# Optimization experiments

Hardware: AMD Instinct MI355X
Metric: run time of the kernel (lower is better)

## Reference

```python
import jax, jax.numpy as jnp
import numpy as np

B, L, DK, DV, H = 2, 2048, 512, 512, 8
DH_K = DK // H  # 64
DH_V = DV // H  # 64


def setup_inputs() -> dict:
    key = jax.random.key(0)
    ks = jax.random.split(key, 6)
    scale_w = 1.0 / np.sqrt(DK)
    return {
        "keys": jax.random.normal(ks[0], (B, L, DK), dtype=jnp.float32),
        "queries": jax.random.normal(ks[1], (B, L, DK), dtype=jnp.float32),
        "values": jax.random.normal(ks[2], (B, L, DV), dtype=jnp.float32),
        "WQ": jax.random.normal(ks[3], (H, DK, DH_K), dtype=jnp.float32) * scale_w,
        "WK": jax.random.normal(ks[4], (H, DK, DH_K), dtype=jnp.float32) * scale_w,
        "WV": jax.random.normal(ks[5], (H, DV, DH_V), dtype=jnp.float32) * scale_w,
    }


def reference(keys, queries, values, WQ, WK, WV):
    # Per-head projections, vectorized over all H heads at once.
    Q = jnp.einsum('bld,hde->bhle', queries, WQ)   # [B,H,Lq,dh]
    K = jnp.einsum('bld,hde->bhle', keys, WK)      # [B,H,Lk,dh]
    V = jnp.einsum('bld,hde->bhle', values, WV)    # [B,H,Lk,dv_h]
    Lk = keys.shape[1]
    # NOTE: original scales by sqrt(seq_len_k), not sqrt(head_dim).
    y = jnp.einsum('bhqe,bhke->bhqk', Q, K) / jnp.sqrt(jnp.float32(Lk))
    # NOTE: original applies softmax over torch dim=1 of [B,Lq,Lk],
    # i.e. the QUERY axis (axis=2 here in [B,H,Lq,Lk]).
    z = jax.nn.softmax(y, axis=2)
    out = jnp.einsum('bhqk,bhke->bhqe', z, V)      # [B,H,Lq,dv_h]
    # Concat heads on the feature dim (same order as torch.concat(..., 2)).
    Bq, Hh, Lq, Dh = out.shape
    return out.transpose(0, 2, 1, 3).reshape(Bq, Lq, Hh * Dh)
```

## Files before the change

### kernel.cpp

```cpp
#include <hip/hip_runtime.h>
#include <hip/hip_bf16.h>

#define LL 2048
#define DM 512
#define SCALE 0.02209708691207961f

typedef unsigned short u16;
typedef __attribute__((ext_vector_type(8))) short short8;
typedef __attribute__((ext_vector_type(4))) short short4v;
typedef __attribute__((ext_vector_type(4))) float f32x4;

#define XAQ_OFF 0u
#define XAK_OFF 2097152u
#define XAV_OFF 4194304u
#define WB_OFF  6291456u
#define QA_OFF  7077888u
#define KA_OFF  9175040u
#define VB_OFF  11272192u
#define S_OFF   13369344u

__device__ __forceinline__ u16 f2bf(float f) {
  union { float f; unsigned u; } v; v.f = f;
  unsigned r = v.u + 0x7fff + ((v.u >> 16) & 1);
  return (u16)(r >> 16);
}
__device__ __forceinline__ size_t frag_idx(int bh, int t64, int w, int c, int lane) {
  return ((((size_t)(bh * 32 + t64) * 4 + w) * 2 + c) * 64 + lane) * 8;
}
__device__ __forceinline__ size_t vb_idx(int bh, int kt, int w, int et, int lane) {
  return ((((size_t)(bh * 32 + kt) * 4 + w) * 4 + et) * 64 + lane) * 4;
}

__global__ __launch_bounds__(256) void prep_kernel(
    const float* __restrict__ queries, const float* __restrict__ keys,
    const float* __restrict__ values, const float* __restrict__ WQ,
    const float* __restrict__ WK, const float* __restrict__ WV,
    u16* __restrict__ wsb) {
  int t = threadIdx.x;
  int blk = blockIdx.x;
  if (blk < 768) {
    int tens = blk >> 8;
    int grp  = blk & 255;
    const float* src = (tens == 0 ? queries : tens == 1 ? keys : values) +
                       (size_t)grp * 16 * 512;
    __shared__ __align__(16) u16 Xs[16][520];
#pragma unroll
    for (int rep = 0; rep < 8; ++rep) {
      int f4 = t + rep * 256;
      int row = f4 >> 7, c4 = f4 & 127;
      float4 v = *(const float4*)(src + (size_t)row * 512 + c4 * 4);
      short4v o;
      o[0] = (short)f2bf(v.x); o[1] = (short)f2bf(v.y);
      o[2] = (short)f2bf(v.z); o[3] = (short)f2bf(v.w);
      *(short4v*)&Xs[row][c4 * 4] = o;
    }
    __syncthreads();
    u16* dst = wsb + (tens == 0 ? XAQ_OFF : tens == 1 ? XAK_OFF : XAV_OFF) +
               (size_t)grp * 16 * 64 * 8;
#pragma unroll
    for (int rep = 0; rep < 4; ++rep) {
      int o = t + rep * 256;
      int kt = o >> 6, lane = o & 63;
      int quad = lane >> 4, l16 = lane & 15;
      short8 v = *(const short8*)&Xs[l16][kt * 32 + quad * 8];
      *(short8*)(dst + (size_t)o * 8) = v;
    }
  } else {
    int c2 = (blk - 768) * 256 + t;
    int lane = c2 & 63;
    int nt = (c2 >> 6) & 3;
    int kt = (c2 >> 8) & 15;
    int h  = (c2 >> 12) & 7;
    int z  = c2 >> 15;
    int quad = lane >> 4, l16 = lane & 15;
    const float* W = (z == 0) ? WQ : (z == 1) ? WK : WV;
    const float* src = W + ((size_t)h * DM + kt * 32 + quad * 8) * 64 + nt * 16 + l16;
    short8 o;
#pragma unroll
    for (int j = 0; j < 8; ++j) o[j] = (short)f2bf(src[(size_t)j * 64]);
    *(short8*)(wsb + WB_OFF + (size_t)c2 * 8) = o;
  }
}

__global__ __launch_bounds__(256) void proj_kernel(u16* __restrict__ wsb) {
  int t = threadIdx.x;
  int lane = t & 63, w = t >> 6, quad = lane >> 4, l16 = lane & 15;
  int z = blockIdx.z, bh = blockIdx.y, b = bh >> 3, h = bh & 7;
  int QT = blockIdx.x;

  const u16* Bw = wsb + WB_OFF + ((size_t)(z * 8 + h) * 16) * 4 * 64 * 8;
  const u16* Ab = wsb + (z == 0 ? XAQ_OFF : z == 1 ? XAK_OFF : XAV_OFF) +
      (((size_t)b * 128 + QT * 4 + w) * 16) * 64 * 8;

  f32x4 acc[4];
#pragma unroll
  for (int nt = 0; nt < 4; ++nt) acc[nt] = (f32x4){0.f, 0.f, 0.f, 0.f};

#pragma unroll 4
  for (int kt = 0; kt < 16; ++kt) {
    short8 a = *(const short8*)(Ab + ((size_t)kt * 64 + lane) * 8);
#pragma unroll
    for (int nt = 0; nt < 4; ++nt) {
      short8 bb = *(const short8*)(Bw + (((size_t)kt * 4 + nt) * 64 + lane) * 8);
      acc[nt] = __builtin_amdgcn_mfma_f32_16x16x32_bf16(a, bb, acc[nt], 0, 0, 0);
    }
  }

  __shared__ float Cs[64][68];
  float sc = (z == 0) ? SCALE : 1.0f;
#pragma unroll
  for (int nt = 0; nt < 4; ++nt)
#pragma unroll
    for (int r = 0; r < 4; ++r)
      Cs[w * 16 + quad * 4 + r][nt * 16 + l16] = acc[nt][r] * sc;
  __syncthreads();

  if (z < 2) {
    u16* base = wsb + (z == 0 ? QA_OFF : KA_OFF);
#pragma unroll
    for (int c = 0; c < 2; ++c) {
      const float* srcr = &Cs[w * 16 + l16][c * 32 + quad * 8];
      short8 o;
#pragma unroll
      for (int j = 0; j < 8; ++j) o[j] = (short)f2bf(srcr[j]);
      *(short8*)(base + frag_idx(bh, QT, w, c, lane)) = o;
    }
  } else {
#pragma unroll
    for (int et = 0; et < 4; ++et) {
      short4v o;
#pragma unroll
      for (int j = 0; j < 4; ++j)
        o[j] = (short)f2bf(Cs[w * 16 + quad * 4 + j][et * 16 + l16]);
      *(short4v*)(wsb + VB_OFF + vb_idx(bh, QT, w, et, lane)) = o;
    }
  }
}

__global__ __launch_bounds__(256) void stats_kernel(u16* __restrict__ wsb) {
  int t = threadIdx.x;
  int lane = t & 63, w = t >> 6, quad = lane >> 4, l16 = lane & 15;
  int bh = blockIdx.x;
  int KT = blockIdx.y;

  short8 ka[4][2];
#pragma unroll
  for (int mt = 0; mt < 4; ++mt)
#pragma unroll
    for (int c = 0; c < 2; ++c)
      ka[mt][c] = *(const short8*)(wsb + KA_OFF + frag_idx(bh, KT, mt, c, lane));

  float rs[4][4];
#pragma unroll
  for (int mt = 0; mt < 4; ++mt)
#pragma unroll
    for (int r = 0; r < 4; ++r) rs[mt][r] = 0.f;

  for (int qt = 0; qt < 32; ++qt) {
    short8 qb0 = *(const short8*)(wsb + QA_OFF + frag_idx(bh, qt, w, 0, lane));
    short8 qb1 = *(const short8*)(wsb + QA_OFF + frag_idx(bh, qt, w, 1, lane));
#pragma unroll
    for (int mt = 0; mt < 4; ++mt) {
      f32x4 y = (f32x4){0.f, 0.f, 0.f, 0.f};
      y = __builtin_amdgcn_mfma_f32_16x16x32_bf16(ka[mt][0], qb0, y, 0, 0, 0);
      y = __builtin_amdgcn_mfma_f32_16x16x32_bf16(ka[mt][1], qb1, y, 0, 0, 0);
#pragma unroll
      for (int r = 0; r < 4; ++r) rs[mt][r] += __expf(y[r]);
    }
  }
#pragma unroll
  for (int mt = 0; mt < 4; ++mt)
#pragma unroll
    for (int r = 0; r < 4; ++r) {
      rs[mt][r] += __shfl_xor(rs[mt][r], 1);
      rs[mt][r] += __shfl_xor(rs[mt][r], 2);
      rs[mt][r] += __shfl_xor(rs[mt][r], 4);
      rs[mt][r] += __shfl_xor(rs[mt][r], 8);
    }

  __shared__ float Sred[4][64];
  if (l16 == 0) {
#pragma unroll
    for (int mt = 0; mt < 4; ++mt)
#pragma unroll
      for (int r = 0; r < 4; ++r)
        Sred[w][mt * 16 + quad * 4 + r] = rs[mt][r];
  }
  __syncthreads();
  if (t < 64) {
    float s = Sred[0][t] + Sred[1][t] + Sred[2][t] + Sred[3][t];
    float* S = (float*)(wsb + S_OFF);
    S[(size_t)bh * LL + KT * 64 + t] = 1.0f / s;
  }
}

__global__ __launch_bounds__(256, 2) void attn_kernel(const u16* __restrict__ wsb,
                                                      float* __restrict__ out) {
  int t = threadIdx.x;
  int lane = t & 63, w = t >> 6, quad = lane >> 4, l16 = lane & 15;
  int bh = blockIdx.x, b = bh >> 3, h = bh & 7;
  int QT = blockIdx.y, qbase = QT * 64;
  const float* S = (const float*)(wsb + S_OFF) + (size_t)bh * LL;

  short8 qf[4][2];
#pragma unroll
  for (int nt = 0; nt < 4; ++nt)
#pragma unroll
    for (int c = 0; c < 2; ++c)
      qf[nt][c] = *(const short8*)(wsb + QA_OFF + frag_idx(bh, QT, nt, c, lane));

  f32x4 oacc[4][4];
#pragma unroll
  for (int nt = 0; nt < 4; ++nt)
#pragma unroll
    for (int et = 0; et < 4; ++et) oacc[nt][et] = (f32x4){0.f, 0.f, 0.f, 0.f};

  for (int kt = 0; kt < 32; ++kt) {
    short8 ka0 = *(const short8*)(wsb + KA_OFF + frag_idx(bh, kt, w, 0, lane));
    short8 ka1 = *(const short8*)(wsb + KA_OFF + frag_idx(bh, kt, w, 1, lane));
    short4v vb[4];
#pragma unroll
    for (int et = 0; et < 4; ++et)
      vb[et] = *(const short4v*)(wsb + VB_OFF + vb_idx(bh, kt, w, et, lane));
    float4 s4 = *(const float4*)(S + kt * 64 + w * 16 + quad * 4);

#pragma unroll
    for (int nt = 0; nt < 4; ++nt) {
      f32x4 y = (f32x4){0.f, 0.f, 0.f, 0.f};
      y = __builtin_amdgcn_mfma_f32_16x16x32_bf16(ka0, qf[nt][0], y, 0, 0, 0);
      y = __builtin_amdgcn_mfma_f32_16x16x32_bf16(ka1, qf[nt][1], y, 0, 0, 0);
      short4v pa;
      pa[0] = (short)f2bf(__expf(y[0]) * s4.x);
      pa[1] = (short)f2bf(__expf(y[1]) * s4.y);
      pa[2] = (short)f2bf(__expf(y[2]) * s4.z);
      pa[3] = (short)f2bf(__expf(y[3]) * s4.w);
#pragma unroll
      for (int et = 0; et < 4; ++et)
        oacc[nt][et] = __builtin_amdgcn_mfma_f32_16x16x16bf16_1k(pa, vb[et], oacc[nt][et], 0, 0, 0);
    }
  }

  __shared__ float red[4][64][68];
#pragma unroll
  for (int nt = 0; nt < 4; ++nt)
#pragma unroll
    for (int et = 0; et < 4; ++et)
#pragma unroll
      for (int r = 0; r < 4; ++r)
        red[w][nt * 16 + quad * 4 + r][et * 16 + l16] = oacc[nt][et][r];
  __syncthreads();
  float* og = out + ((size_t)b * LL + qbase + w * 16) * 512 + h * 64;
#pragma unroll
  for (int i = 0; i < 16; ++i) {
    float s = red[0][w * 16 + i][lane] + red[1][w * 16 + i][lane] +
              red[2][w * 16 + i][lane] + red[3][w * 16 + i][lane];
    og[(size_t)i * 512 + lane] = s;
  }
}

extern "C" void kernel_launch(void* const* d_in, const int* in_sizes, int n_in,
                              void* d_out, int out_size, void* d_ws, size_t ws_size,
                              hipStream_t stream) {
  const float* keys    = (const float*)d_in[0];
  const float* queries = (const float*)d_in[1];
  const float* values  = (const float*)d_in[2];
  const float* WQ      = (const float*)d_in[3];
  const float* WK      = (const float*)d_in[4];
  const float* WV      = (const float*)d_in[5];
  float* out = (float*)d_out;
  u16* wsb = (u16*)d_ws;

  prep_kernel<<<dim3(1152), 256, 0, stream>>>(queries, keys, values, WQ, WK, WV, wsb);
  proj_kernel<<<dim3(32, 16, 3), 256, 0, stream>>>(wsb);
  stats_kernel<<<dim3(16, 32), 256, 0, stream>>>(wsb);
  attn_kernel<<<dim3(16, 32), 256, 0, stream>>>(wsb, out);
}
```

Before: 139.0 us.

## Prefetch next tile operands, fold log2e into Q scale, use exp2 and setprio

Folds log2(e) into the Q projection scale so both attention kernels can call the hardware exp2 instruction directly instead of __expf. The column-sum and output loops now load the next tile's Q/K/V fragments and S values into registers while computing the current tile. s_setprio is raised around MFMA groups to favour matrix issue across waves. The prefetch uses more registers, which can lower occupancy, and the last iteration wraps around to load tile 0 again, which is redundant work.

```diff
diff --git a/kernel.cpp b/kernel.cpp
--- a/kernel.cpp
+++ b/kernel.cpp
@@ -3,7 +3,7 @@
 
 #define LL 2048
 #define DM 512
-#define SCALE 0.02209708691207961f
+#define SCALE2 0.031879357f
 
 typedef unsigned short u16;
 typedef __attribute__((ext_vector_type(8))) short short8;
@@ -107,7 +107,7 @@
   }
 
   __shared__ float Cs[64][68];
-  float sc = (z == 0) ? SCALE : 1.0f;
+  float sc = (z == 0) ? SCALE2 : 1.0f;
 #pragma unroll
   for (int nt = 0; nt < 4; ++nt)
 #pragma unroll
@@ -156,17 +156,23 @@
 #pragma unroll
     for (int r = 0; r < 4; ++r) rs[mt][r] = 0.f;
 
+  short8 qb0 = *(const short8*)(wsb + QA_OFF + frag_idx(bh, 0, w, 0, lane));
+  short8 qb1 = *(const short8*)(wsb + QA_OFF + frag_idx(bh, 0, w, 1, lane));
   for (int qt = 0; qt < 32; ++qt) {
-    short8 qb0 = *(const short8*)(wsb + QA_OFF + frag_idx(bh, qt, w, 0, lane));
-    short8 qb1 = *(const short8*)(wsb + QA_OFF + frag_idx(bh, qt, w, 1, lane));
+    int qn = (qt + 1) & 31;
+    short8 nq0 = *(const short8*)(wsb + QA_OFF + frag_idx(bh, qn, w, 0, lane));
+    short8 nq1 = *(const short8*)(wsb + QA_OFF + frag_idx(bh, qn, w, 1, lane));
 #pragma unroll
     for (int mt = 0; mt < 4; ++mt) {
       f32x4 y = (f32x4){0.f, 0.f, 0.f, 0.f};
+      __builtin_amdgcn_s_setprio(1);
       y = __builtin_amdgcn_mfma_f32_16x16x32_bf16(ka[mt][0], qb0, y, 0, 0, 0);
       y = __builtin_amdgcn_mfma_f32_16x16x32_bf16(ka[mt][1], qb1, y, 0, 0, 0);
-#pragma unroll
-      for (int r = 0; r < 4; ++r) rs[mt][r] += __expf(y[r]);
-    }
+      __builtin_amdgcn_s_setprio(0);
+#pragma unroll
+      for (int r = 0; r < 4; ++r) rs[mt][r] += __builtin_amdgcn_exp2f(y[r]);
+    }
+    qb0 = nq0; qb1 = nq1;
   }
 #pragma unroll
   for (int mt = 0; mt < 4; ++mt)
@@ -215,29 +221,50 @@
 #pragma unroll
     for (int et = 0; et < 4; ++et) oacc[nt][et] = (f32x4){0.f, 0.f, 0.f, 0.f};
 
+  short8 ka0 = *(const short8*)(wsb + KA_OFF + frag_idx(bh, 0, w, 0, lane));
+  short8 ka1 = *(const short8*)(wsb + KA_OFF + frag_idx(bh, 0, w, 1, lane));
+  short4v vb[4];
+#pragma unroll
+  for (int et = 0; et < 4; ++et)
+    vb[et] = *(const short4v*)(wsb + VB_OFF + vb_idx(bh, 0, w, et, lane));
+  float4 s4 = *(const float4*)(S + w * 16 + quad * 4);
+
   for (int kt = 0; kt < 32; ++kt) {
-    short8 ka0 = *(const short8*)(wsb + KA_OFF + frag_idx(bh, kt, w, 0, lane));
-    short8 ka1 = *(const short8*)(wsb + KA_OFF + frag_idx(bh, kt, w, 1, lane));
-    short4v vb[4];
+    int kn = (kt + 1) & 31;
+    short8 nka0 = *(const short8*)(wsb + KA_OFF + frag_idx(bh, kn, w, 0, lane));
+    short8 nka1 = *(const short8*)(wsb + KA_OFF + frag_idx(bh, kn, w, 1, lane));
+    short4v nvb[4];
 #pragma unroll
     for (int et = 0; et < 4; ++et)
-      vb[et] = *(const short4v*)(wsb + VB_OFF + vb_idx(bh, kt, w, et, lane));
-    float4 s4 = *(const float4*)(S + kt * 64 + w * 16 + quad * 4);
+      nvb[et] = *(const short4v*)(wsb + VB_OFF + vb_idx(bh, kn, w, et, lane));
+    float4 ns4 = *(const float4*)(S + kn * 64 + w * 16 + quad * 4);
 
 #pragma unroll
     for (int nt = 0; nt < 4; ++nt) {
       f32x4 y = (f32x4){0.f, 0.f, 0.f, 0.f};
+      __builtin_amdgcn_s_setprio(1);
       y = __builtin_amdgcn_mfma_f32_16x16x32_bf16(ka0, qf[nt][0], y, 0, 0, 0);
       y = __builtin_amdgcn_mfma_f32_16x16x32_bf16(ka1, qf[nt][1], y, 0, 0, 0);
+      __builtin_amdgcn_s_setprio(0);
+      float e0 = __builtin_amdgcn_exp2f(y[0]) * s4.x;
+      float e1 = __builtin_amdgcn_exp2f(y[1]) * s4.y;
+      float e2 = __builtin_amdgcn_exp2f(y[2]) * s4.z;
+      float e3 = __builtin_amdgcn_exp2f(y[3]) * s4.w;
       short4v pa;
-      pa[0] = (short)f2bf(__expf(y[0]) * s4.x);
-      pa[1] = (short)f2bf(__expf(y[1]) * s4.y);
-      pa[2] = (short)f2bf(__expf(y[2]) * s4.z);
-      pa[3] = (short)f2bf(__expf(y[3]) * s4.w);
+      pa[0] = (short)f2bf(e0);
+      pa[1] = (short)f2bf(e1);
+      pa[2] = (short)f2bf(e2);
+      pa[3] = (short)f2bf(e3);
+      __builtin_amdgcn_s_setprio(1);
 #pragma unroll
       for (int et = 0; et < 4; ++et)
         oacc[nt][et] = __builtin_amdgcn_mfma_f32_16x16x16bf16_1k(pa, vb[et], oacc[nt][et], 0, 0, 0);
-    }
+      __builtin_amdgcn_s_setprio(0);
+    }
+    ka0 = nka0; ka1 = nka1;
+#pragma unroll
+    for (int et = 0; et < 4; ++et) vb[et] = nvb[et];
+    s4 = ns4;
   }
 
   __shared__ float red[4][64][68];
```

Result: no change. 138.1 us (-0.7%).

## Software-pipeline stats and attention loops with triple-buffered register prefetch and K=32 PV MFMA

Applied to the files above, without the earlier changes.

The stats and attention loops now prefetch Q/K/V fragments and the softmax normalizers three stages ahead into rotating register sets, so global loads overlap with MFMA work. The attention kernel processes two key tiles per step and uses the 16x16x32 bf16 MFMA for P·V, which requires a new interleaved V fragment layout written by the prep kernel. The Q scale now folds in log2(e) so exp2 can replace expf. Wave priority hints are set around the MFMA groups. The extra register sets raise VGPR pressure under the two-blocks-per-SM launch bound, which could cause spills.

```diff
diff --git a/kernel.cpp b/kernel.cpp
--- a/kernel.cpp
+++ b/kernel.cpp
@@ -3,7 +3,7 @@
 
 #define LL 2048
 #define DM 512
-#define SCALE 0.02209708691207961f
+#define SCALE2 0.031879357f
 
 typedef unsigned short u16;
 typedef __attribute__((ext_vector_type(8))) short short8;
@@ -27,8 +27,8 @@
 __device__ __forceinline__ size_t frag_idx(int bh, int t64, int w, int c, int lane) {
   return ((((size_t)(bh * 32 + t64) * 4 + w) * 2 + c) * 64 + lane) * 8;
 }
-__device__ __forceinline__ size_t vb_idx(int bh, int kt, int w, int et, int lane) {
-  return ((((size_t)(bh * 32 + kt) * 4 + w) * 4 + et) * 64 + lane) * 4;
+__device__ __forceinline__ size_t vb8_idx(int bh, int kt2, int w, int et, int lane) {
+  return ((((size_t)(bh * 16 + kt2) * 4 + w) * 4 + et) * 64 + lane) * 8;
 }
 
 __global__ __launch_bounds__(256) void prep_kernel(
@@ -107,7 +107,7 @@
   }
 
   __shared__ float Cs[64][68];
-  float sc = (z == 0) ? SCALE : 1.0f;
+  float sc = (z == 0) ? SCALE2 : 1.0f;
 #pragma unroll
   for (int nt = 0; nt < 4; ++nt)
 #pragma unroll
@@ -132,10 +132,26 @@
 #pragma unroll
       for (int j = 0; j < 4; ++j)
         o[j] = (short)f2bf(Cs[w * 16 + quad * 4 + j][et * 16 + l16]);
-      *(short4v*)(wsb + VB_OFF + vb_idx(bh, QT, w, et, lane)) = o;
-    }
-  }
-}
+      *(short4v*)(wsb + VB_OFF + vb8_idx(bh, QT >> 1, w, et, lane) + (QT & 1) * 4) = o;
+    }
+  }
+}
+
+#define STATS_PHASE(QB0, QB1, QNEW)                                             \
+  {                                                                             \
+    _Pragma("unroll")                                                           \
+    for (int mt = 0; mt < 4; ++mt) {                                            \
+      f32x4 y = (f32x4){0.f, 0.f, 0.f, 0.f};                                    \
+      __builtin_amdgcn_s_setprio(1);                                            \
+      y = __builtin_amdgcn_mfma_f32_16x16x32_bf16(ka[mt][0], QB0, y, 0, 0, 0);  \
+      y = __builtin_amdgcn_mfma_f32_16x16x32_bf16(ka[mt][1], QB1, y, 0, 0, 0);  \
+      __builtin_amdgcn_s_setprio(0);                                            \
+      _Pragma("unroll")                                                         \
+      for (int r = 0; r < 4; ++r) rs[mt][r] += __builtin_amdgcn_exp2f(y[r]);    \
+    }                                                                           \
+    QB0 = *(const short8*)(wsb + QA_OFF + frag_idx(bh, (QNEW) & 31, w, 0, lane)); \
+    QB1 = *(const short8*)(wsb + QA_OFF + frag_idx(bh, (QNEW) & 31, w, 1, lane)); \
+  }
 
 __global__ __launch_bounds__(256) void stats_kernel(u16* __restrict__ wsb) {
   int t = threadIdx.x;
@@ -156,18 +172,23 @@
 #pragma unroll
     for (int r = 0; r < 4; ++r) rs[mt][r] = 0.f;
 
-  for (int qt = 0; qt < 32; ++qt) {
-    short8 qb0 = *(const short8*)(wsb + QA_OFF + frag_idx(bh, qt, w, 0, lane));
-    short8 qb1 = *(const short8*)(wsb + QA_OFF + frag_idx(bh, qt, w, 1, lane));
-#pragma unroll
-    for (int mt = 0; mt < 4; ++mt) {
-      f32x4 y = (f32x4){0.f, 0.f, 0.f, 0.f};
-      y = __builtin_amdgcn_mfma_f32_16x16x32_bf16(ka[mt][0], qb0, y, 0, 0, 0);
-      y = __builtin_amdgcn_mfma_f32_16x16x32_bf16(ka[mt][1], qb1, y, 0, 0, 0);
-#pragma unroll
-      for (int r = 0; r < 4; ++r) rs[mt][r] += __expf(y[r]);
-    }
-  }
+  short8 qA0 = *(const short8*)(wsb + QA_OFF + frag_idx(bh, 0, w, 0, lane));
+  short8 qA1 = *(const short8*)(wsb + QA_OFF + frag_idx(bh, 0, w, 1, lane));
+  short8 qB0 = *(const short8*)(wsb + QA_OFF + frag_idx(bh, 1, w, 0, lane));
+  short8 qB1 = *(const short8*)(wsb + QA_OFF + frag_idx(bh, 1, w, 1, lane));
+  short8 qC0 = *(const short8*)(wsb + QA_OFF + frag_idx(bh, 2, w, 0, lane));
+  short8 qC1 = *(const short8*)(wsb + QA_OFF + frag_idx(bh, 2, w, 1, lane));
+
+#pragma unroll 1
+  for (int j = 0; j < 10; ++j) {
+    int k0 = 3 * j;
+    STATS_PHASE(qA0, qA1, k0 + 3);
+    STATS_PHASE(qB0, qB1, k0 + 4);
+    STATS_PHASE(qC0, qC1, k0 + 5);
+  }
+  STATS_PHASE(qA0, qA1, 0);
+  STATS_PHASE(qB0, qB1, 0);
+
 #pragma unroll
   for (int mt = 0; mt < 4; ++mt)
 #pragma unroll
@@ -193,6 +214,62 @@
     S[(size_t)bh * LL + KT * 64 + t] = 1.0f / s;
   }
 }
+
+#define ATTN_PHASE(KE0, KE1, KO0, KO1, VBX, S4E, S4O, KNEW)                         \
+  {                                                                                 \
+    _Pragma("unroll")                                                               \
+    for (int nt = 0; nt < 4; ++nt) {                                                \
+      f32x4 ye = (f32x4){0.f, 0.f, 0.f, 0.f};                                       \
+      f32x4 yo = (f32x4){0.f, 0.f, 0.f, 0.f};                                       \
+      __builtin_amdgcn_s_setprio(1);                                                \
+      ye = __builtin_amdgcn_mfma_f32_16x16x32_bf16(KE0, qf[nt][0], ye, 0, 0, 0);    \
+      ye = __builtin_amdgcn_mfma_f32_16x16x32_bf16(KE1, qf[nt][1], ye, 0, 0, 0);    \
+      yo = __builtin_amdgcn_mfma_f32_16x16x32_bf16(KO0, qf[nt][0], yo, 0, 0, 0);    \
+      yo = __builtin_amdgcn_mfma_f32_16x16x32_bf16(KO1, qf[nt][1], yo, 0, 0, 0);    \
+      __builtin_amdgcn_s_setprio(0);                                                \
+      short8 pa8;                                                                   \
+      pa8[0] = (short)f2bf(__builtin_amdgcn_exp2f(ye[0]) * S4E.x);                  \
+      pa8[1] = (short)f2bf(__builtin_amdgcn_exp2f(ye[1]) * S4E.y);                  \
+      pa8[2] = (short)f2bf(__builtin_amdgcn_exp2f(ye[2]) * S4E.z);                  \
+      pa8[3] = (short)f2bf(__builtin_amdgcn_exp2f(ye[3]) * S4E.w);                  \
+      pa8[4] = (short)f2bf(__builtin_amdgcn_exp2f(yo[0]) * S4O.x);                  \
+      pa8[5] = (short)f2bf(__builtin_amdgcn_exp2f(yo[1]) * S4O.y);                  \
+      pa8[6] = (short)f2bf(__builtin_amdgcn_exp2f(yo[2]) * S4O.z);                  \
+      pa8[7] = (short)f2bf(__builtin_amdgcn_exp2f(yo[3]) * S4O.w);                  \
+      __builtin_amdgcn_s_setprio(1);                                                \
+      _Pragma("unroll")                                                             \
+      for (int et = 0; et < 4; ++et)                                                \
+        oacc[nt][et] = __builtin_amdgcn_mfma_f32_16x16x32_bf16(pa8, VBX[et],        \
+                                                               oacc[nt][et], 0, 0, 0); \
+      __builtin_amdgcn_s_setprio(0);                                                \
+    }                                                                               \
+    {                                                                               \
+      int ke = (2 * (KNEW)) & 31, ko = (2 * (KNEW) + 1) & 31, kv = (KNEW) & 15;     \
+      KE0 = *(const short8*)(wsb + KA_OFF + frag_idx(bh, ke, w, 0, lane));          \
+      KE1 = *(const short8*)(wsb + KA_OFF + frag_idx(bh, ke, w, 1, lane));          \
+      KO0 = *(const short8*)(wsb + KA_OFF + frag_idx(bh, ko, w, 0, lane));          \
+      KO1 = *(const short8*)(wsb + KA_OFF + frag_idx(bh, ko, w, 1, lane));          \
+      _Pragma("unroll")                                                             \
+      for (int et = 0; et < 4; ++et)                                                \
+        VBX[et] = *(const short8*)(wsb + VB_OFF + vb8_idx(bh, kv, w, et, lane));    \
+      S4E = *(const float4*)(S + ke * 64 + w * 16 + quad * 4);                      \
+      S4O = *(const float4*)(S + ko * 64 + w * 16 + quad * 4);                      \
+    }                                                                               \
+  }
+
+#define ATTN_LOADSET(KE0, KE1, KO0, KO1, VBX, S4E, S4O, KT2)                        \
+  {                                                                                 \
+    int ke = 2 * (KT2), ko = 2 * (KT2) + 1;                                         \
+    KE0 = *(const short8*)(wsb + KA_OFF + frag_idx(bh, ke, w, 0, lane));            \
+    KE1 = *(const short8*)(wsb + KA_OFF + frag_idx(bh, ke, w, 1, lane));            \
+    KO0 = *(const short8*)(wsb + KA_OFF + frag_idx(bh, ko, w, 0, lane));            \
+    KO1 = *(const short8*)(wsb + KA_OFF + frag_idx(bh, ko, w, 1, lane));            \
+    _Pragma("unroll")                                                               \
+    for (int et = 0; et < 4; ++et)                                                  \
+      VBX[et] = *(const short8*)(wsb + VB_OFF + vb8_idx(bh, (KT2), w, et, lane));   \
+    S4E = *(const float4*)(S + ke * 64 + w * 16 + quad * 4);                        \
+    S4O = *(const float4*)(S + ko * 64 + w * 16 + quad * 4);                        \
+  }
 
 __global__ __launch_bounds__(256, 2) void attn_kernel(const u16* __restrict__ wsb,
                                                       float* __restrict__ out) {
@@ -215,30 +292,21 @@
 #pragma unroll
     for (int et = 0; et < 4; ++et) oacc[nt][et] = (f32x4){0.f, 0.f, 0.f, 0.f};
 
-  for (int kt = 0; kt < 32; ++kt) {
-    short8 ka0 = *(const short8*)(wsb + KA_OFF + frag_idx(bh, kt, w, 0, lane));
-    short8 ka1 = *(const short8*)(wsb + KA_OFF + frag_idx(bh, kt, w, 1, lane));
-    short4v vb[4];
-#pragma unroll
-    for (int et = 0; et < 4; ++et)
-      vb[et] = *(const short4v*)(wsb + VB_OFF + vb_idx(bh, kt, w, et, lane));
-    float4 s4 = *(const float4*)(S + kt * 64 + w * 16 + quad * 4);
-
-#pragma unroll
-    for (int nt = 0; nt < 4; ++nt) {
-      f32x4 y = (f32x4){0.f, 0.f, 0.f, 0.f};
-      y = __builtin_amdgcn_mfma_f32_16x16x32_bf16(ka0, qf[nt][0], y, 0, 0, 0);
-      y = __builtin_amdgcn_mfma_f32_16x16x32_bf16(ka1, qf[nt][1], y, 0, 0, 0);
-      short4v pa;
-      pa[0] = (short)f2bf(__expf(y[0]) * s4.x);
-      pa[1] = (short)f2bf(__expf(y[1]) * s4.y);
-      pa[2] = (short)f2bf(__expf(y[2]) * s4.z);
-      pa[3] = (short)f2bf(__expf(y[3]) * s4.w);
-#pragma unroll
-      for (int et = 0; et < 4; ++et)
-        oacc[nt][et] = __builtin_amdgcn_mfma_f32_16x16x16bf16_1k(pa, vb[et], oacc[nt][et], 0, 0, 0);
-    }
-  }
+  short8 aKE0, aKE1, aKO0, aKO1, aVB[4]; float4 aSE, aSO;
+  short8 bKE0, bKE1, bKO0, bKO1, bVB[4]; float4 bSE, bSO;
+  short8 cKE0, cKE1, cKO0, cKO1, cVB[4]; float4 cSE, cSO;
+  ATTN_LOADSET(aKE0, aKE1, aKO0, aKO1, aVB, aSE, aSO, 0)
+  ATTN_LOADSET(bKE0, bKE1, bKO0, bKO1, bVB, bSE, bSO, 1)
+  ATTN_LOADSET(cKE0, cKE1, cKO0, cKO1, cVB, cSE, cSO, 2)
+
+#pragma unroll 1
+  for (int j = 0; j < 5; ++j) {
+    int k0 = 3 * j;
+    ATTN_PHASE(aKE0, aKE1, aKO0, aKO1, aVB, aSE, aSO, k0 + 3)
+    ATTN_PHASE(bKE0, bKE1, bKO0, bKO1, bVB, bSE, bSO, k0 + 4)
+    ATTN_PHASE(cKE0, cKE1, cKO0, cKO1, cVB, cSE, cSO, k0 + 5)
+  }
+  ATTN_PHASE(aKE0, aKE1, aKO0, aKO1, aVB, aSE, aSO, 0)
 
   __shared__ float red[4][64][68];
 #pragma unroll
```

Measured after the change: 135.2 us. 2.7% less time.
